# Optimization experiments

Hardware: AMD Instinct MI355X
Metric: run time of the kernel (lower is better)

The kernel has to match this reference:

```python
import jax, jax.numpy as jnp
import numpy as np

B, D, H = 4096, 1024, 1024

def _glorot(key, shape):
    fan_in, fan_out = shape
    limit = np.sqrt(6.0 / (fan_in + fan_out))
    return jax.random.uniform(key, shape, jnp.float32, -limit, limit)

def setup_inputs() -> dict:
    key = jax.random.key(0)
    ks = jax.random.split(key, 12)
    inp = {
        'inputs': jax.random.normal(ks[0], (B, D), jnp.float32),
        'h_prev': jax.random.normal(ks[1], (B, H), jnp.float32),
        'c_prev': jax.random.normal(ks[2], (B, H), jnp.float32),
    }
    names = ['f', 'i', 'c', 'o']
    for j, n in enumerate(names):
        inp['W_' + n] = _glorot(ks[3 + 2 * j], (D, H))
        inp['U_' + n] = _glorot(ks[4 + 2 * j], (H, H))
        inp['b_' + n] = jnp.zeros((H,), jnp.float32)
    return inp

def reference(inputs, h_prev, c_prev, W_f, U_f, b_f, W_i, U_i, b_i, W_c, U_c, b_c, W_o, U_o, b_o):
    f_t = jax.nn.sigmoid(inputs @ W_f + h_prev @ U_f + b_f)
    i_t = jax.nn.sigmoid(inputs @ W_i + h_prev @ U_i + b_i)
    c_tilde = jnp.tanh(inputs @ W_c + h_prev @ U_c + b_c)
    c_next = f_t * c_prev + i_t * c_tilde
    o_t = jax.nn.sigmoid(inputs @ W_o + h_prev @ U_o + b_o)
    h_next = o_t * jnp.tanh(c_next)
    return (h_next, c_next)
```

## Files before the change

kernel.cpp:

```cpp
#include <hip/hip_runtime.h>


typedef __attribute__((ext_vector_type(8))) short bfrag8;

__device__ __forceinline__ unsigned int f2bf(float f) {
  unsigned int u = __builtin_bit_cast(unsigned int, f);
  unsigned int r = (u + 0x7fffu + ((u >> 16) & 1u)) >> 16;
  return r & 0xffffu;
}

__global__ __launch_bounds__(256) void prep_x(const float* __restrict__ inputs,
                                              const float* __restrict__ h_prev,
                                              unsigned short* __restrict__ X) {
  int idx = blockIdx.x * 256 + threadIdx.x;
  int b  = idx >> 8;
  int k8 = (idx & 255) * 8;
  const float* src = (k8 < 1024) ? (inputs + (size_t)b * 1024 + k8)
                                 : (h_prev + (size_t)b * 1024 + (k8 - 1024));
  float4 v0 = ((const float4*)src)[0];
  float4 v1 = ((const float4*)src)[1];
  uint4 o;
  o.x = f2bf(v0.x) | (f2bf(v0.y) << 16);
  o.y = f2bf(v0.z) | (f2bf(v0.w) << 16);
  o.z = f2bf(v1.x) | (f2bf(v1.y) << 16);
  o.w = f2bf(v1.z) | (f2bf(v1.w) << 16);
  *(uint4*)(X + (size_t)b * 2048 + k8) = o;
}

__global__ __launch_bounds__(256) void prep_w(
    const float* __restrict__ s0, const float* __restrict__ s1,
    const float* __restrict__ s2, const float* __restrict__ s3,
    const float* __restrict__ s4, const float* __restrict__ s5,
    const float* __restrict__ s6, const float* __restrict__ s7,
    unsigned short* __restrict__ Wct) {
  int blk = blockIdx.x;
  int m = blk >> 8;
  const float* src = (m == 0) ? s0 : (m == 1) ? s1 : (m == 2) ? s2 : (m == 3) ? s3
                   : (m == 4) ? s4 : (m == 5) ? s5 : (m == 6) ? s6 : s7;
  int g = m >> 1, half = m & 1;
  unsigned short* dst = Wct + (size_t)g * 1024 * 2048 + (size_t)half * 1024;
  int t = blk & 255;
  int k0 = (t >> 4) * 64;
  int h0 = (t & 15) * 64;
  __shared__ float lt[64][68];
  int tid = threadIdx.x;
  #pragma unroll
  for (int it = 0; it < 4; ++it) {
    int r  = (tid >> 4) + it * 16;
    int c4 = (tid & 15) * 4;
    float4 v = *(const float4*)(src + (size_t)(k0 + r) * 1024 + h0 + c4);
    lt[r][c4 + 0] = v.x; lt[r][c4 + 1] = v.y; lt[r][c4 + 2] = v.z; lt[r][c4 + 3] = v.w;
  }
  __syncthreads();
  #pragma unroll
  for (int it = 0; it < 4; ++it) {
    int hh  = (tid >> 4) + it * 16;
    int kk4 = (tid & 15) * 4;
    uint2 o;
    o.x = f2bf(lt[kk4 + 0][hh]) | (f2bf(lt[kk4 + 1][hh]) << 16);
    o.y = f2bf(lt[kk4 + 2][hh]) | (f2bf(lt[kk4 + 3][hh]) << 16);
    *(uint2*)(dst + (size_t)(h0 + hh) * 2048 + k0 + kk4) = o;
  }
}


#define FENCE() asm volatile("" ::: "memory")
#define BARRIER() do { FENCE(); __builtin_amdgcn_s_barrier(); FENCE(); } while (0)
#define VMCNT0() asm volatile("s_waitcnt vmcnt(0)" ::: "memory")
#define LGKM0() asm volatile("s_waitcnt lgkmcnt(0)" ::: "memory")
#define GLOAD16(gp, lp) __builtin_amdgcn_global_load_lds( \
    (const __attribute__((address_space(1))) unsigned int*)(gp), \
    (__attribute__((address_space(3))) unsigned int*)(lp), 16, 0, 0)
#define DSR(dst, addr, off) asm volatile("ds_read_b128 %0, %1 offset:%c2" \
    : "=v"(dst) : "v"(addr), "n"(off))

#define AC "a0","a1","a2","a3","a4","a5","a6","a7","a8","a9","a10","a11","a12","a13","a14","a15", \
 "a16","a17","a18","a19","a20","a21","a22","a23","a24","a25","a26","a27","a28","a29","a30","a31", \
 "a32","a33","a34","a35","a36","a37","a38","a39","a40","a41","a42","a43","a44","a45","a46","a47", \
 "a48","a49","a50","a51","a52","a53","a54","a55","a56","a57","a58","a59","a60","a61","a62","a63"

#define WZ(n) "v_accvgpr_write_b32 a" #n ", 0\n\t"
#define AINIT() asm volatile( \
 WZ(0)WZ(1)WZ(2)WZ(3)WZ(4)WZ(5)WZ(6)WZ(7)WZ(8)WZ(9)WZ(10)WZ(11)WZ(12)WZ(13)WZ(14)WZ(15) \
 WZ(16)WZ(17)WZ(18)WZ(19)WZ(20)WZ(21)WZ(22)WZ(23)WZ(24)WZ(25)WZ(26)WZ(27)WZ(28)WZ(29)WZ(30)WZ(31) \
 WZ(32)WZ(33)WZ(34)WZ(35)WZ(36)WZ(37)WZ(38)WZ(39)WZ(40)WZ(41)WZ(42)WZ(43)WZ(44)WZ(45)WZ(46)WZ(47) \
 WZ(48)WZ(49)WZ(50)WZ(51)WZ(52)WZ(53)WZ(54)WZ(55)WZ(56)WZ(57)WZ(58)WZ(59)WZ(60)WZ(61)WZ(62)WZ(63) \
 ::: AC)

#define MFMA_ONE(BR, AF, BF) asm volatile( \
    "v_mfma_f32_16x16x32_bf16 a[" BR "], %0, %1, a[" BR "]" \
    :: "v"(AF), "v"(BF) : AC)

#define CL16() do { \
  __builtin_amdgcn_s_setprio(1); \
  MFMA_ONE("0:3",   Af[0], Bf[0]); MFMA_ONE("4:7",   Af[1], Bf[0]); \
  MFMA_ONE("8:11",  Af[2], Bf[0]); MFMA_ONE("12:15", Af[3], Bf[0]); \
  MFMA_ONE("16:19", Af[0], Bf[1]); MFMA_ONE("20:23", Af[1], Bf[1]); \
  MFMA_ONE("24:27", Af[2], Bf[1]); MFMA_ONE("28:31", Af[3], Bf[1]); \
  MFMA_ONE("32:35", Af[0], Bf[2]); MFMA_ONE("36:39", Af[1], Bf[2]); \
  MFMA_ONE("40:43", Af[2], Bf[2]); MFMA_ONE("44:47", Af[3], Bf[2]); \
  MFMA_ONE("48:51", Af[0], Bf[3]); MFMA_ONE("52:55", Af[1], Bf[3]); \
  MFMA_ONE("56:59", Af[2], Bf[3]); MFMA_ONE("60:63", Af[3], Bf[3]); \
  __builtin_amdgcn_s_setprio(0); \
} while (0)

#define READ_A(BUF) do { \
  DSR(Af[0], aAb, (BUF)*16384 + 0);    \
  DSR(Af[1], aAb, (BUF)*16384 + 1024); \
  DSR(Af[2], aAb, (BUF)*16384 + 2048); \
  DSR(Af[3], aAb, (BUF)*16384 + 3072); \
} while (0)

#define READ_B(BUF) do { \
  DSR(Bf[0], aBb, (BUF)*8192 + 0);    \
  DSR(Bf[1], aBb, (BUF)*8192 + 1024); \
  DSR(Bf[2], aBb, (BUF)*8192 + 2048); \
  DSR(Bf[3], aBb, (BUF)*8192 + 3072); \
} while (0)

#define STAGE(BUF, kt) do { int _kb = ((kt) < 64 ? (kt) : 63) * 32; \
  GLOAD16(pA0 + _kb, smem + (BUF)*16384 + stb); \
  GLOAD16(pA1 + _kb, smem + (BUF)*16384 + 8192 + stb); \
  GLOAD16(pBs + _kb, smem + 32768 + (BUF)*8192 + stb); \
} while (0)

#define ARD(X, RS) asm volatile("v_accvgpr_read_b32 %0, " RS : "=v"(X))

#define EPI_M(Mi, F0,F1,F2,F3, I0,I1,I2,I3, C0,C1,C2,C3, O0,O1,O2,O3) do { \
  float pf[4], pi[4], pc[4], po[4]; \
  ARD(pf[0],F0); ARD(pf[1],F1); ARD(pf[2],F2); ARD(pf[3],F3); \
  ARD(pi[0],I0); ARD(pi[1],I1); ARD(pi[2],I2); ARD(pi[3],I3); \
  ARD(pc[0],C0); ARD(pc[1],C1); ARD(pc[2],C2); ARD(pc[3],C3); \
  ARD(po[0],O0); ARD(po[1],O1); ARD(po[2],O2); ARD(po[3],O3); \
  _Pragma("unroll") for (int j = 0; j < 4; ++j) { \
    const int b = rbw + (Mi) * 16 + q * 4 + j; \
    float xf = pf[j] + Bgf, xi = pi[j] + Bgi, xc = pc[j] + Bgc, xo = po[j] + Bgo; \
    float fg = 1.f / (1.f + __expf(-xf)); \
    float ig = 1.f / (1.f + __expf(-xi)); \
    float ct = 2.f / (1.f + __expf(-2.f * xc)) - 1.f; \
    float og = 1.f / (1.f + __expf(-xo)); \
    float cn = fg * c_prev[(size_t)b * 1024 + hcol] + ig * ct; \
    float hn = og * (2.f / (1.f + __expf(-2.f * cn)) - 1.f); \
    out[(size_t)b * 1024 + hcol] = hn; \
    out[(size_t)4194304 + (size_t)b * 1024 + hcol] = cn; \
  } \
} while (0)

__global__ __launch_bounds__(512, 4) void lstm_gemm(
    const unsigned short* __restrict__ X, const unsigned short* __restrict__ Wct,
    const float* __restrict__ c_prev,
    const float* __restrict__ bfv, const float* __restrict__ biv,
    const float* __restrict__ bcv, const float* __restrict__ bov,
    float* __restrict__ out) {
  extern __shared__ __align__(16) char smem[];
  const int tid = threadIdx.x;
  const int lane = tid & 63, w = tid >> 6;
  const int u = lane & 15, q = (lane >> 4) & 3;
  const int wm = w >> 1, wn = w & 1;

  const int bid = blockIdx.x;
  const int swz = (bid & 7) * 64 + (bid >> 3);
  const int row0 = (swz >> 5) * 256;
  const int h0 = (swz & 31) * 32;

  const unsigned lds0 = (unsigned)(size_t)((__attribute__((address_space(3))) char*)smem);

  const int fsw = (q ^ ((u >> 1) & 3)) << 4;
  const unsigned aAb = lds0 + (wm * 64 + u) * 64 + fsw;
  const unsigned aBb = lds0 + 32768 + (wn * 64 + u) * 64 + fsw;

  const int stb = tid * 16;
  const int srow = tid >> 2;
  const int sg = (tid & 3) ^ ((tid >> 3) & 3);
  const unsigned short* pA0 = X + (size_t)(row0 + srow) * 2048 + sg * 8;
  const unsigned short* pA1 = X + (size_t)(row0 + 128 + srow) * 2048 + sg * 8;
  const int bg = (srow >> 4) & 3;
  const int wr = bg * 1024 + h0 + (srow >> 6) * 16 + (srow & 15);
  const unsigned short* pBs = Wct + (size_t)wr * 2048 + sg * 8;

  AINIT();
  bfrag8 Af[4], Bf[4];

  STAGE(0, 0);
  VMCNT0();
  BARRIER();

  #pragma unroll 1
  for (int tt = 0; tt < 32; ++tt) {
    const int t1 = 2 * tt + 1, t2 = 2 * tt + 2;
    READ_A(0); READ_B(0);
    STAGE(1, t1);
    LGKM0();
    CL16();
    VMCNT0();
    BARRIER();
    READ_A(1); READ_B(1);
    STAGE(0, t2);
    LGKM0();
    CL16();
    VMCNT0();
    BARRIER();
  }
  asm volatile("s_nop 7\n\ts_nop 7");

  const int hcol = h0 + wn * 16 + u;
  const float Bgf = bfv[hcol], Bgi = biv[hcol], Bgc = bcv[hcol], Bgo = bov[hcol];
  const int rbw = row0 + wm * 64;
  EPI_M(0, "a0","a1","a2","a3",     "a16","a17","a18","a19",
           "a32","a33","a34","a35", "a48","a49","a50","a51");
  EPI_M(1, "a4","a5","a6","a7",     "a20","a21","a22","a23",
           "a36","a37","a38","a39", "a52","a53","a54","a55");
  EPI_M(2, "a8","a9","a10","a11",   "a24","a25","a26","a27",
           "a40","a41","a42","a43", "a56","a57","a58","a59");
  EPI_M(3, "a12","a13","a14","a15", "a28","a29","a30","a31",
           "a44","a45","a46","a47", "a60","a61","a62","a63");
}

extern "C" void kernel_launch(void* const* d_in, const int* in_sizes, int n_in,
                              void* d_out, int out_size, void* d_ws, size_t ws_size,
                              hipStream_t stream) {
  const float* inputs = (const float*)d_in[0];
  const float* h_prev = (const float*)d_in[1];
  const float* c_prev = (const float*)d_in[2];
  const float* Wf = (const float*)d_in[3];
  const float* Uf = (const float*)d_in[4];
  const float* bf = (const float*)d_in[5];
  const float* Wi = (const float*)d_in[6];
  const float* Ui = (const float*)d_in[7];
  const float* bi = (const float*)d_in[8];
  const float* Wc = (const float*)d_in[9];
  const float* Uc = (const float*)d_in[10];
  const float* bc = (const float*)d_in[11];
  const float* Wo = (const float*)d_in[12];
  const float* Uo = (const float*)d_in[13];
  const float* bo = (const float*)d_in[14];
  float* out = (float*)d_out;

  unsigned short* X   = (unsigned short*)d_ws;
  unsigned short* Wct = X + (size_t)4096 * 2048;

  (void)hipFuncSetAttribute(reinterpret_cast<const void*>(lstm_gemm),
                            hipFuncAttributeMaxDynamicSharedMemorySize, 49152);

  prep_x<<<4096, 256, 0, stream>>>(inputs, h_prev, X);
  prep_w<<<2048, 256, 0, stream>>>(Wf, Uf, Wi, Ui, Wc, Uc, Wo, Uo, Wct);
  lstm_gemm<<<512, 512, 49152, stream>>>(X, Wct, c_prev, bf, bi, bc, bo, out);
}
```

Before: 101.1 us.

## Merge prep kernels and double per-wave GEMM tile with 256-thread blocks

Merges the activation and weight bf16 conversion kernels into one launch, which removes one launch and its inter-kernel gap. The GEMM now uses 4 waves per block instead of 8, with each wave computing a 128x16-per-gate tile (128 accumulator registers, 8 A fragments), which roughly halves LDS reads per MFMA. Block-to-tile mapping is changed so each XCD covers two adjacent row blocks. The cost is higher register pressure, fewer waves for latency hiding, and more global-to-LDS loads per thread.

After: 102.4 us. Within noise of the previous version (+1.3%).

```diff
diff --git a/kernel.cpp b/kernel.cpp
--- a/kernel.cpp
+++ b/kernel.cpp
@@ -9,31 +9,32 @@
   return r & 0xffffu;
 }
 
-__global__ __launch_bounds__(256) void prep_x(const float* __restrict__ inputs,
-                                              const float* __restrict__ h_prev,
-                                              unsigned short* __restrict__ X) {
-  int idx = blockIdx.x * 256 + threadIdx.x;
-  int b  = idx >> 8;
-  int k8 = (idx & 255) * 8;
-  const float* src = (k8 < 1024) ? (inputs + (size_t)b * 1024 + k8)
-                                 : (h_prev + (size_t)b * 1024 + (k8 - 1024));
-  float4 v0 = ((const float4*)src)[0];
-  float4 v1 = ((const float4*)src)[1];
-  uint4 o;
-  o.x = f2bf(v0.x) | (f2bf(v0.y) << 16);
-  o.y = f2bf(v0.z) | (f2bf(v0.w) << 16);
-  o.z = f2bf(v1.x) | (f2bf(v1.y) << 16);
-  o.w = f2bf(v1.z) | (f2bf(v1.w) << 16);
-  *(uint4*)(X + (size_t)b * 2048 + k8) = o;
-}
-
-__global__ __launch_bounds__(256) void prep_w(
+__global__ __launch_bounds__(256) void prep_all(
+    const float* __restrict__ inputs, const float* __restrict__ h_prev,
     const float* __restrict__ s0, const float* __restrict__ s1,
     const float* __restrict__ s2, const float* __restrict__ s3,
     const float* __restrict__ s4, const float* __restrict__ s5,
     const float* __restrict__ s6, const float* __restrict__ s7,
-    unsigned short* __restrict__ Wct) {
-  int blk = blockIdx.x;
+    unsigned short* __restrict__ X, unsigned short* __restrict__ Wct) {
+  const int bidAll = blockIdx.x;
+  const int tid = threadIdx.x;
+  if (bidAll < 4096) {
+    int idx = bidAll * 256 + tid;
+    int b  = idx >> 8;
+    int k8 = (idx & 255) * 8;
+    const float* src = (k8 < 1024) ? (inputs + (size_t)b * 1024 + k8)
+                                   : (h_prev + (size_t)b * 1024 + (k8 - 1024));
+    float4 v0 = ((const float4*)src)[0];
+    float4 v1 = ((const float4*)src)[1];
+    uint4 o;
+    o.x = f2bf(v0.x) | (f2bf(v0.y) << 16);
+    o.y = f2bf(v0.z) | (f2bf(v0.w) << 16);
+    o.z = f2bf(v1.x) | (f2bf(v1.y) << 16);
+    o.w = f2bf(v1.z) | (f2bf(v1.w) << 16);
+    *(uint4*)(X + (size_t)b * 2048 + k8) = o;
+    return;
+  }
+  int blk = bidAll - 4096;
   int m = blk >> 8;
   const float* src = (m == 0) ? s0 : (m == 1) ? s1 : (m == 2) ? s2 : (m == 3) ? s3
                    : (m == 4) ? s4 : (m == 5) ? s5 : (m == 6) ? s6 : s7;
@@ -43,7 +44,6 @@
   int k0 = (t >> 4) * 64;
   int h0 = (t & 15) * 64;
   __shared__ float lt[64][68];
-  int tid = threadIdx.x;
   #pragma unroll
   for (int it = 0; it < 4; ++it) {
     int r  = (tid >> 4) + it * 16;
@@ -77,7 +77,11 @@
 #define AC "a0","a1","a2","a3","a4","a5","a6","a7","a8","a9","a10","a11","a12","a13","a14","a15", \
  "a16","a17","a18","a19","a20","a21","a22","a23","a24","a25","a26","a27","a28","a29","a30","a31", \
  "a32","a33","a34","a35","a36","a37","a38","a39","a40","a41","a42","a43","a44","a45","a46","a47", \
- "a48","a49","a50","a51","a52","a53","a54","a55","a56","a57","a58","a59","a60","a61","a62","a63"
+ "a48","a49","a50","a51","a52","a53","a54","a55","a56","a57","a58","a59","a60","a61","a62","a63", \
+ "a64","a65","a66","a67","a68","a69","a70","a71","a72","a73","a74","a75","a76","a77","a78","a79", \
+ "a80","a81","a82","a83","a84","a85","a86","a87","a88","a89","a90","a91","a92","a93","a94","a95", \
+ "a96","a97","a98","a99","a100","a101","a102","a103","a104","a105","a106","a107","a108","a109","a110","a111", \
+ "a112","a113","a114","a115","a116","a117","a118","a119","a120","a121","a122","a123","a124","a125","a126","a127"
 
 #define WZ(n) "v_accvgpr_write_b32 a" #n ", 0\n\t"
 #define AINIT() asm volatile( \
@@ -85,43 +89,56 @@
  WZ(16)WZ(17)WZ(18)WZ(19)WZ(20)WZ(21)WZ(22)WZ(23)WZ(24)WZ(25)WZ(26)WZ(27)WZ(28)WZ(29)WZ(30)WZ(31) \
  WZ(32)WZ(33)WZ(34)WZ(35)WZ(36)WZ(37)WZ(38)WZ(39)WZ(40)WZ(41)WZ(42)WZ(43)WZ(44)WZ(45)WZ(46)WZ(47) \
  WZ(48)WZ(49)WZ(50)WZ(51)WZ(52)WZ(53)WZ(54)WZ(55)WZ(56)WZ(57)WZ(58)WZ(59)WZ(60)WZ(61)WZ(62)WZ(63) \
+ WZ(64)WZ(65)WZ(66)WZ(67)WZ(68)WZ(69)WZ(70)WZ(71)WZ(72)WZ(73)WZ(74)WZ(75)WZ(76)WZ(77)WZ(78)WZ(79) \
+ WZ(80)WZ(81)WZ(82)WZ(83)WZ(84)WZ(85)WZ(86)WZ(87)WZ(88)WZ(89)WZ(90)WZ(91)WZ(92)WZ(93)WZ(94)WZ(95) \
+ WZ(96)WZ(97)WZ(98)WZ(99)WZ(100)WZ(101)WZ(102)WZ(103)WZ(104)WZ(105)WZ(106)WZ(107)WZ(108)WZ(109)WZ(110)WZ(111) \
+ WZ(112)WZ(113)WZ(114)WZ(115)WZ(116)WZ(117)WZ(118)WZ(119)WZ(120)WZ(121)WZ(122)WZ(123)WZ(124)WZ(125)WZ(126)WZ(127) \
  ::: AC)
 
 #define MFMA_ONE(BR, AF, BF) asm volatile( \
     "v_mfma_f32_16x16x32_bf16 a[" BR "], %0, %1, a[" BR "]" \
     :: "v"(AF), "v"(BF) : AC)
 
-#define CL16() do { \
+#define CL32() do { \
   __builtin_amdgcn_s_setprio(1); \
-  MFMA_ONE("0:3",   Af[0], Bf[0]); MFMA_ONE("4:7",   Af[1], Bf[0]); \
-  MFMA_ONE("8:11",  Af[2], Bf[0]); MFMA_ONE("12:15", Af[3], Bf[0]); \
-  MFMA_ONE("16:19", Af[0], Bf[1]); MFMA_ONE("20:23", Af[1], Bf[1]); \
-  MFMA_ONE("24:27", Af[2], Bf[1]); MFMA_ONE("28:31", Af[3], Bf[1]); \
-  MFMA_ONE("32:35", Af[0], Bf[2]); MFMA_ONE("36:39", Af[1], Bf[2]); \
-  MFMA_ONE("40:43", Af[2], Bf[2]); MFMA_ONE("44:47", Af[3], Bf[2]); \
-  MFMA_ONE("48:51", Af[0], Bf[3]); MFMA_ONE("52:55", Af[1], Bf[3]); \
-  MFMA_ONE("56:59", Af[2], Bf[3]); MFMA_ONE("60:63", Af[3], Bf[3]); \
+  MFMA_ONE("0:3",    Af[0], Bf[0]); MFMA_ONE("4:7",    Af[1], Bf[0]); \
+  MFMA_ONE("8:11",   Af[2], Bf[0]); MFMA_ONE("12:15",  Af[3], Bf[0]); \
+  MFMA_ONE("16:19",  Af[4], Bf[0]); MFMA_ONE("20:23",  Af[5], Bf[0]); \
+  MFMA_ONE("24:27",  Af[6], Bf[0]); MFMA_ONE("28:31",  Af[7], Bf[0]); \
+  MFMA_ONE("32:35",  Af[0], Bf[1]); MFMA_ONE("36:39",  Af[1], Bf[1]); \
+  MFMA_ONE("40:43",  Af[2], Bf[1]); MFMA_ONE("44:47",  Af[3], Bf[1]); \
+  MFMA_ONE("48:51",  Af[4], Bf[1]); MFMA_ONE("52:55",  Af[5], Bf[1]); \
+  MFMA_ONE("56:59",  Af[6], Bf[1]); MFMA_ONE("60:63",  Af[7], Bf[1]); \
+  MFMA_ONE("64:67",  Af[0], Bf[2]); MFMA_ONE("68:71",  Af[1], Bf[2]); \
+  MFMA_ONE("72:75",  Af[2], Bf[2]); MFMA_ONE("76:79",  Af[3], Bf[2]); \
+  MFMA_ONE("80:83",  Af[4], Bf[2]); MFMA_ONE("84:87",  Af[5], Bf[2]); \
+  MFMA_ONE("88:91",  Af[6], Bf[2]); MFMA_ONE("92:95",  Af[7], Bf[2]); \
+  MFMA_ONE("96:99",  Af[0], Bf[3]); MFMA_ONE("100:103",Af[1], Bf[3]); \
+  MFMA_ONE("104:107",Af[2], Bf[3]); MFMA_ONE("108:111",Af[3], Bf[3]); \
+  MFMA_ONE("112:115",Af[4], Bf[3]); MFMA_ONE("116:119",Af[5], Bf[3]); \
+  MFMA_ONE("120:123",Af[6], Bf[3]); MFMA_ONE("124:127",Af[7], Bf[3]); \
   __builtin_amdgcn_s_setprio(0); \
 } while (0)
 
 #define READ_A(BUF) do { \
-  DSR(Af[0], aAb, (BUF)*16384 + 0);    \
-  DSR(Af[1], aAb, (BUF)*16384 + 1024); \
-  DSR(Af[2], aAb, (BUF)*16384 + 2048); \
-  DSR(Af[3], aAb, (BUF)*16384 + 3072); \
+  DSR(Af[0], aA, (BUF)*16384 + 0);    DSR(Af[1], aA, (BUF)*16384 + 1024); \
+  DSR(Af[2], aA, (BUF)*16384 + 2048); DSR(Af[3], aA, (BUF)*16384 + 3072); \
+  DSR(Af[4], aA, (BUF)*16384 + 4096); DSR(Af[5], aA, (BUF)*16384 + 5120); \
+  DSR(Af[6], aA, (BUF)*16384 + 6144); DSR(Af[7], aA, (BUF)*16384 + 7168); \
 } while (0)
 
 #define READ_B(BUF) do { \
-  DSR(Bf[0], aBb, (BUF)*8192 + 0);    \
-  DSR(Bf[1], aBb, (BUF)*8192 + 1024); \
-  DSR(Bf[2], aBb, (BUF)*8192 + 2048); \
-  DSR(Bf[3], aBb, (BUF)*8192 + 3072); \
+  DSR(Bf[0], aB, (BUF)*8192 + 0);    DSR(Bf[1], aB, (BUF)*8192 + 1024); \
+  DSR(Bf[2], aB, (BUF)*8192 + 2048); DSR(Bf[3], aB, (BUF)*8192 + 3072); \
 } while (0)
 
 #define STAGE(BUF, kt) do { int _kb = ((kt) < 64 ? (kt) : 63) * 32; \
-  GLOAD16(pA0 + _kb, smem + (BUF)*16384 + stb); \
-  GLOAD16(pA1 + _kb, smem + (BUF)*16384 + 8192 + stb); \
-  GLOAD16(pBs + _kb, smem + 32768 + (BUF)*8192 + stb); \
+  GLOAD16(pA0 + _kb, smem + (BUF)*16384 + dA0); \
+  GLOAD16(pA1 + _kb, smem + (BUF)*16384 + dA1); \
+  GLOAD16(pA2 + _kb, smem + (BUF)*16384 + dA2); \
+  GLOAD16(pA3 + _kb, smem + (BUF)*16384 + dA3); \
+  GLOAD16(pB0 + _kb, smem + 32768 + (BUF)*8192 + dB0); \
+  GLOAD16(pB1 + _kb, smem + 32768 + (BUF)*8192 + dB1); \
 } while (0)
 
 #define ARD(X, RS) asm volatile("v_accvgpr_read_b32 %0, " RS : "=v"(X))
@@ -146,7 +163,7 @@
   } \
 } while (0)
 
-__global__ __launch_bounds__(512, 4) void lstm_gemm(
+__global__ __launch_bounds__(256, 2) void lstm_gemm(
     const unsigned short* __restrict__ X, const unsigned short* __restrict__ Wct,
     const float* __restrict__ c_prev,
     const float* __restrict__ bfv, const float* __restrict__ biv,
@@ -159,27 +176,33 @@
   const int wm = w >> 1, wn = w & 1;
 
   const int bid = blockIdx.x;
-  const int swz = (bid & 7) * 64 + (bid >> 3);
-  const int row0 = (swz >> 5) * 256;
-  const int h0 = (swz & 31) * 32;
+  const int xcd = bid & 7, idx = bid >> 3;
+  const int row0 = (xcd * 2 + (idx & 1)) * 256;
+  const int h0 = (idx >> 1) * 32;
 
   const unsigned lds0 = (unsigned)(size_t)((__attribute__((address_space(3))) char*)smem);
 
   const int fsw = (q ^ ((u >> 1) & 3)) << 4;
-  const unsigned aAb = lds0 + (wm * 64 + u) * 64 + fsw;
-  const unsigned aBb = lds0 + 32768 + (wn * 64 + u) * 64 + fsw;
-
-  const int stb = tid * 16;
-  const int srow = tid >> 2;
-  const int sg = (tid & 3) ^ ((tid >> 3) & 3);
-  const unsigned short* pA0 = X + (size_t)(row0 + srow) * 2048 + sg * 8;
-  const unsigned short* pA1 = X + (size_t)(row0 + 128 + srow) * 2048 + sg * 8;
-  const int bg = (srow >> 4) & 3;
-  const int wr = bg * 1024 + h0 + (srow >> 6) * 16 + (srow & 15);
-  const unsigned short* pBs = Wct + (size_t)wr * 2048 + sg * 8;
+  const unsigned aA = lds0 + (wm * 128 + u) * 64 + fsw;
+  const unsigned aB = lds0 + 32768 + (wn * 64 + u) * 64 + fsw;
+
+  const int l4 = lane >> 2;
+  const int ss = (lane & 3) ^ ((l4 >> 1) & 3);
+  const int sA0 = 0 * 4 + w, sA1 = 1 * 4 + w, sA2 = 2 * 4 + w, sA3 = 3 * 4 + w;
+  const int sB0 = 0 * 4 + w, sB1 = 1 * 4 + w;
+  const int dA0 = sA0 * 1024 + lane * 16, dA1 = sA1 * 1024 + lane * 16;
+  const int dA2 = sA2 * 1024 + lane * 16, dA3 = sA3 * 1024 + lane * 16;
+  const int dB0 = sB0 * 1024 + lane * 16, dB1 = sB1 * 1024 + lane * 16;
+  const unsigned short* pA0 = X + (size_t)(row0 + sA0 * 16 + l4) * 2048 + ss * 8;
+  const unsigned short* pA1 = X + (size_t)(row0 + sA1 * 16 + l4) * 2048 + ss * 8;
+  const unsigned short* pA2 = X + (size_t)(row0 + sA2 * 16 + l4) * 2048 + ss * 8;
+  const unsigned short* pA3 = X + (size_t)(row0 + sA3 * 16 + l4) * 2048 + ss * 8;
+  auto wrow = [&](int C) { return (((C >> 4) & 3) << 10) + h0 + ((C >> 6) << 4) + (C & 15); };
+  const unsigned short* pB0 = Wct + (size_t)wrow(sB0 * 16 + l4) * 2048 + ss * 8;
+  const unsigned short* pB1 = Wct + (size_t)wrow(sB1 * 16 + l4) * 2048 + ss * 8;
 
   AINIT();
-  bfrag8 Af[4], Bf[4];
+  bfrag8 Af[8], Bf[4];
 
   STAGE(0, 0);
   VMCNT0();
@@ -191,29 +214,38 @@
     READ_A(0); READ_B(0);
     STAGE(1, t1);
     LGKM0();
-    CL16();
+    CL32();
     VMCNT0();
     BARRIER();
     READ_A(1); READ_B(1);
     STAGE(0, t2);
     LGKM0();
-    CL16();
+    CL32();
     VMCNT0();
     BARRIER();
   }
+  LGKM0();
   asm volatile("s_nop 7\n\ts_nop 7");
 
   const int hcol = h0 + wn * 16 + u;
   const float Bgf = bfv[hcol], Bgi = biv[hcol], Bgc = bcv[hcol], Bgo = bov[hcol];
-  const int rbw = row0 + wm * 64;
-  EPI_M(0, "a0","a1","a2","a3",     "a16","a17","a18","a19",
-           "a32","a33","a34","a35", "a48","a49","a50","a51");
-  EPI_M(1, "a4","a5","a6","a7",     "a20","a21","a22","a23",
-           "a36","a37","a38","a39", "a52","a53","a54","a55");
-  EPI_M(2, "a8","a9","a10","a11",   "a24","a25","a26","a27",
-           "a40","a41","a42","a43", "a56","a57","a58","a59");
-  EPI_M(3, "a12","a13","a14","a15", "a28","a29","a30","a31",
-           "a44","a45","a46","a47", "a60","a61","a62","a63");
+  const int rbw = row0 + wm * 128;
+  EPI_M(0, "a0","a1","a2","a3",     "a32","a33","a34","a35",
+           "a64","a65","a66","a67", "a96","a97","a98","a99");
+  EPI_M(1, "a4","a5","a6","a7",     "a36","a37","a38","a39",
+           "a68","a69","a70","a71", "a100","a101","a102","a103");
+  EPI_M(2, "a8","a9","a10","a11",   "a40","a41","a42","a43",
+           "a72","a73","a74","a75", "a104","a105","a106","a107");
+  EPI_M(3, "a12","a13","a14","a15", "a44","a45","a46","a47",
+           "a76","a77","a78","a79", "a108","a109","a110","a111");
+  EPI_M(4, "a16","a17","a18","a19", "a48","a49","a50","a51",
+           "a80","a81","a82","a83", "a112","a113","a114","a115");
+  EPI_M(5, "a20","a21","a22","a23", "a52","a53","a54","a55",
+           "a84","a85","a86","a87", "a116","a117","a118","a119");
+  EPI_M(6, "a24","a25","a26","a27", "a56","a57","a58","a59",
+           "a88","a89","a90","a91", "a120","a121","a122","a123");
+  EPI_M(7, "a28","a29","a30","a31", "a60","a61","a62","a63",
+           "a92","a93","a94","a95", "a124","a125","a126","a127");
 }
 
 extern "C" void kernel_launch(void* const* d_in, const int* in_sizes, int n_in,
@@ -242,7 +274,7 @@
   (void)hipFuncSetAttribute(reinterpret_cast<const void*>(lstm_gemm),
                             hipFuncAttributeMaxDynamicSharedMemorySize, 49152);
 
-  prep_x<<<4096, 256, 0, stream>>>(inputs, h_prev, X);
-  prep_w<<<2048, 256, 0, stream>>>(Wf, Uf, Wi, Ui, Wc, Uc, Wo, Uo, Wct);
-  lstm_gemm<<<512, 512, 49152, stream>>>(X, Wct, c_prev, bf, bi, bc, bo, out);
-}
+  prep_all<<<6144, 256, 0, stream>>>(inputs, h_prev,
+                                     Wf, Uf, Wi, Ui, Wc, Uc, Wo, Uo, X, Wct);
+  lstm_gemm<<<512, 256, 49152, stream>>>(X, Wct, c_prev, bf, bi, bc, bo, out);
+}
```
